# Kernel optimization log

Measured on AMD Instinct MI355X. Metric: run time of the kernel, lower is better.

The kernel has to match this reference:

```python
import jax, jax.numpy as jnp
import numpy as np

N_NODES = 100000


def gcn_conv(x, W, b, src, dst, n_nodes):
    """PyG GCNConv: add self-loops, symmetric D^-1/2 A D^-1/2 normalization,
    linear transform, gather-scale-scatter aggregation, bias."""
    h = x @ W  # [N, out]
    loops = jnp.arange(n_nodes, dtype=src.dtype)
    s = jnp.concatenate([src, loops])  # sources incl. self-loops
    d = jnp.concatenate([dst, loops])  # targets incl. self-loops
    deg = jax.ops.segment_sum(jnp.ones_like(d, dtype=h.dtype), d,
                              num_segments=n_nodes)  # in-degree (+1 self loop)
    dinv = jnp.where(deg > 0, jax.lax.rsqrt(deg), 0.0)
    norm = dinv[s] * dinv[d]  # [E+N]
    msg = h[s] * norm[:, None]  # gather + scale  [E+N, out]
    out = jax.ops.segment_sum(msg, d, num_segments=n_nodes)  # scatter-add
    return out + b


def setup_inputs() -> dict:
    key = jax.random.key(0)
    k1, k2, k3, k4, k5, k6 = jax.random.split(key, 6)
    in_ch, out_ch = 128, 64
    n_edges = 1_600_000
    x = jax.random.normal(k1, (N_NODES, in_ch), dtype=jnp.float32)
    edge_index = jax.random.randint(k2, (2, n_edges), 0, N_NODES, dtype=jnp.int64)
    # Glorot-style init for GCN weights, zero bias (PyG defaults)
    W_enc = jax.random.normal(k3, (in_ch, out_ch), dtype=jnp.float32) * (1.0 / np.sqrt(in_ch))
    b_enc = jnp.zeros((out_ch,), dtype=jnp.float32)
    W_dec = jax.random.normal(k4, (out_ch, in_ch), dtype=jnp.float32) * (1.0 / np.sqrt(out_ch))
    b_dec = jnp.zeros((in_ch,), dtype=jnp.float32)
    return {"x": x, "edge_index": edge_index,
            "W_enc": W_enc, "b_enc": b_enc, "W_dec": W_dec, "b_dec": b_dec}


def reference(x, edge_index, W_enc, b_enc, W_dec, b_dec):
    src, dst = edge_index[0], edge_index[1]
    loc_emb = gcn_conv(x, W_enc, b_enc, src, dst, N_NODES)
    loc_reconstruct = gcn_conv(loc_emb, W_dec, b_dec, src, dst, N_NODES)
    return (loc_emb, loc_reconstruct)
```

## Files before the change

kernel.cpp:

```cpp
#include <hip/hip_runtime.h>
#include <hip/hip_fp16.h>


#define BSHIFT 7
#define BNODES (1 << BSHIFT)
#define NB_LDS 1024

__global__ __launch_bounds__(1024)
void part_kernel(const int* __restrict__ src, const int* __restrict__ dst,
                 int E, int NB, int* __restrict__ gcur, int* __restrict__ gbuf,
                 int BSTRIDE)
{
    __shared__ int hist[NB_LDS];
    __shared__ int bbase[NB_LDS];
    const int tid = threadIdx.x;
    for (int i = tid; i < NB; i += 1024) hist[i] = 0;
    __syncthreads();

    const int base = (blockIdx.x * 1024 + tid) * 4;
    int bk[4], lp[4], pk[4];
    int nv = 0;
    if (base + 4 <= E) {
        const int4 d4 = *reinterpret_cast<const int4*>(dst + base);
        const int4 s4 = *reinterpret_cast<const int4*>(src + base);
        nv = 4;
        #pragma unroll
        for (int k = 0; k < 4; ++k) {
            const int d = (&d4.x)[k];
            bk[k] = d >> BSHIFT;
            pk[k] = ((&s4.x)[k] << BSHIFT) | (d & (BNODES - 1));
            lp[k] = atomicAdd(&hist[bk[k]], 1);
        }
    } else {
        for (int k = 0; base + k < E && k < 4; ++k) {
            const int d = dst[base + k];
            bk[nv] = d >> BSHIFT;
            pk[nv] = (src[base + k] << BSHIFT) | (d & (BNODES - 1));
            lp[nv] = atomicAdd(&hist[bk[nv]], 1);
            ++nv;
        }
    }
    __syncthreads();
    for (int i = tid; i < NB; i += 1024) {
        const int c = hist[i];
        bbase[i] = c ? atomicAdd(&gcur[i], c) : 0;
    }
    __syncthreads();
    for (int k = 0; k < nv; ++k) {
        const int pos = bbase[bk[k]] + lp[k];
        if (pos < BSTRIDE) gbuf[(size_t)bk[k] * BSTRIDE + pos] = pk[k];
    }
}

__global__ __launch_bounds__(256)
void csr_kernel(const int* __restrict__ gcur, const int* __restrict__ gbuf,
                int BSTRIDE, int* __restrict__ csr, int cap,
                int* __restrict__ cnt, float* __restrict__ dinv, int M)
{
    __shared__ int cur[BNODES];
    const int tid = threadIdx.x;
    const int b   = blockIdx.x;
    if (tid < BNODES) cur[tid] = 0;
    __syncthreads();

    int nb = gcur[b];
    if (nb > BSTRIDE) nb = BSTRIDE;
    const int* __restrict__ buf = gbuf + (size_t)b * BSTRIDE;
    const int n0 = b << BSHIFT;

    for (int i = tid; i < nb; i += 256) {
        const int p = buf[i];
        const int d = p & (BNODES - 1);
        const int s = p >> BSHIFT;
        const int lpos = atomicAdd(&cur[d], 1);
        if (lpos < cap) csr[(size_t)(n0 + d) * cap + lpos] = s;
    }
    __syncthreads();
    const int n = n0 + tid;
    if (tid < BNODES && n < M) {
        const int c = cur[tid];
        cnt[n]  = c;
        dinv[n] = rsqrtf((float)c + 1.0f);
    }
}

template<int K, int N, bool HOUT>
__global__ __launch_bounds__(256)
void gemm_scale(const float* __restrict__ X, const float* __restrict__ W,
                const float* __restrict__ dinv, const float* __restrict__ bias,
                float* __restrict__ out, __half* __restrict__ outh, int M)
{
    constexpr int TM  = 64;
    constexpr int QPR = K / 4;
    __shared__ float Ws[K * N];
    __shared__ float Xs[TM * K];

    const int tid  = threadIdx.x;
    const int row0 = blockIdx.x * TM;

    for (int i = tid; i < K * N / 4; i += 256) {
        float4 v = reinterpret_cast<const float4*>(W)[i];
        *reinterpret_cast<float4*>(&Ws[i * 4]) = v;
    }
    for (int i = tid; i < TM * QPR; i += 256) {
        int r = i / QPR, q = i - r * QPR;
        int gr = row0 + r;
        float4 v = make_float4(0.f, 0.f, 0.f, 0.f);
        if (gr < M) v = reinterpret_cast<const float4*>(X)[(size_t)gr * QPR + q];
        *reinterpret_cast<float4*>(&Xs[r * K + q * 4]) = v;
    }
    __syncthreads();

    constexpr int CG  = N / 4;
    constexpr int RPT = N / 16;
    const int c0 = (tid % CG) * 4;
    const int r0 = (tid / CG) * RPT;

    float a[RPT][4];
    #pragma unroll
    for (int rr = 0; rr < RPT; ++rr) {
        a[rr][0] = 0.f; a[rr][1] = 0.f; a[rr][2] = 0.f; a[rr][3] = 0.f;
    }

    #pragma unroll 4
    for (int k = 0; k < K; ++k) {
        const float4 wv = *reinterpret_cast<const float4*>(&Ws[k * N + c0]);
        #pragma unroll
        for (int rr = 0; rr < RPT; ++rr) {
            const float xv = Xs[(r0 + rr) * K + k];
            a[rr][0] += xv * wv.x;
            a[rr][1] += xv * wv.y;
            a[rr][2] += xv * wv.z;
            a[rr][3] += xv * wv.w;
        }
    }

    float4 bv = make_float4(0.f, 0.f, 0.f, 0.f);
    if (bias) bv = *reinterpret_cast<const float4*>(&bias[c0]);

    #pragma unroll
    for (int rr = 0; rr < RPT; ++rr) {
        const int gr = row0 + r0 + rr;
        if (gr < M) {
            const float d = dinv[gr];
            float4 v;
            v.x = a[rr][0] * d + bv.x; v.y = a[rr][1] * d + bv.y;
            v.z = a[rr][2] * d + bv.z; v.w = a[rr][3] * d + bv.w;
            if constexpr (HOUT) {
                union { __half2 h2[2]; uint2 u; } pk;
                pk.h2[0] = __floats2half2_rn(v.x, v.y);
                pk.h2[1] = __floats2half2_rn(v.z, v.w);
                *reinterpret_cast<uint2*>(&outh[(size_t)gr * N + c0]) = pk.u;
            } else {
                *reinterpret_cast<float4*>(&out[(size_t)gr * N + c0]) = v;
            }
        }
    }
}

template<bool FIRST>
__global__ __launch_bounds__(256)
void gcn_agg(const __half* __restrict__ hsh, const int* __restrict__ csr,
             const int* __restrict__ cnt, const float* __restrict__ dinv,
             const float* __restrict__ bias, float* __restrict__ outf,
             __half* __restrict__ outh, int M, int cap)
{
    const int lane = threadIdx.x & 63;
    int n = (blockIdx.x * 256 + threadIdx.x) >> 6;
    if (n >= M) return;
    n = __builtin_amdgcn_readfirstlane(n);
    int deg = cnt[n];
    if (deg > cap) deg = cap;
    const int* __restrict__ lst = csr + (size_t)n * cap;

    float acc = __half2float(hsh[(size_t)n * 64 + lane]);

    int j = 0;
    for (; j + 16 <= deg; j += 16) {
        int   s[16];
        float v[16];
        #pragma unroll
        for (int k = 0; k < 16; ++k) s[k] = lst[j + k];
        #pragma unroll
        for (int k = 0; k < 16; ++k) v[k] = __half2float(hsh[(size_t)s[k] * 64 + lane]);
        float t = 0.f;
        #pragma unroll
        for (int k = 0; k < 16; ++k) t += v[k];
        acc += t;
    }
    for (; j + 4 <= deg; j += 4) {
        const int s0 = lst[j], s1 = lst[j + 1], s2 = lst[j + 2], s3 = lst[j + 3];
        const float v0 = __half2float(hsh[(size_t)s0 * 64 + lane]);
        const float v1 = __half2float(hsh[(size_t)s1 * 64 + lane]);
        const float v2 = __half2float(hsh[(size_t)s2 * 64 + lane]);
        const float v3 = __half2float(hsh[(size_t)s3 * 64 + lane]);
        acc += (v0 + v1) + (v2 + v3);
    }
    for (; j < deg; ++j) acc += __half2float(hsh[(size_t)lst[j] * 64 + lane]);

    if constexpr (FIRST) {
        const float dv = dinv[n];
        const float e  = acc * dv + bias[lane];
        outf[(size_t)n * 64 + lane] = e;
        outh[(size_t)n * 64 + lane] = __float2half_rn(e * dv);
    } else {
        outf[(size_t)n * 64 + lane] = acc;
    }
}

extern "C" void kernel_launch(void* const* d_in, const int* in_sizes, int n_in,
                              void* d_out, int out_size, void* d_ws, size_t ws_size,
                              hipStream_t stream)
{
    const float* x    = (const float*)d_in[0];
    const int*   ei   = (const int*)  d_in[1];
    const float* Wenc = (const float*)d_in[2];
    const float* benc = (const float*)d_in[3];
    const float* Wdec = (const float*)d_in[4];
    const float* bdec = (const float*)d_in[5];

    const int M = in_sizes[0] / 128;
    const int E = in_sizes[1] / 2;
    const int* src  = ei;
    const int* dstv = ei + E;

    float* emb   = (float*)d_out;
    float* recon = (float*)d_out + (size_t)M * 64;

    const int NB      = (M + BNODES - 1) >> BSHIFT;
    const int BSTRIDE = 3072;

    __half* hs1h  = (__half*)d_ws;
    __half* ghalf = (__half*)((int*)d_ws + (size_t)M * 32);
    int*    gbuf  = (int*)d_ws + (size_t)M * 64;
    float*  agg2  = (float*)((int*)d_ws + (size_t)M * 64);
    int*    cnt   = (int*)d_ws + (size_t)M * 128;
    float*  dinv  = (float*)((int*)d_ws + (size_t)M * 129);
    int*    gcur  = (int*)d_ws + (size_t)M * 130;
    int*    csr   = (int*)d_ws + (size_t)M * 130 + 1024;

    const size_t used = ((size_t)M * 130 + 1024) * 4;
    int cap = 64;
    const size_t avail = (ws_size > used) ? (ws_size - used) / ((size_t)M * 4) : 0;
    if ((size_t)cap > avail) cap = (int)avail;

    hipMemsetAsync(gcur, 0, 1024 * sizeof(int), stream);

    part_kernel<<<(E + 4095) / 4096, 1024, 0, stream>>>(src, dstv, E, NB, gcur, gbuf, BSTRIDE);
    csr_kernel<<<NB, 256, 0, stream>>>(gcur, gbuf, BSTRIDE, csr, cap, cnt, dinv, M);

    const int aggBlocks = (M + 3) / 4;

    gemm_scale<128, 64, true><<<(M + 63) / 64, 256, 0, stream>>>(
        x, Wenc, dinv, nullptr, nullptr, hs1h, M);
    gcn_agg<true><<<aggBlocks, 256, 0, stream>>>(
        hs1h, csr, cnt, dinv, benc, emb, ghalf, M, cap);

    gcn_agg<false><<<aggBlocks, 256, 0, stream>>>(
        ghalf, csr, cnt, nullptr, nullptr, agg2, nullptr, M, cap);
    gemm_scale<64, 128, false><<<(M + 63) / 64, 256, 0, stream>>>(
        agg2, Wdec, dinv, bdec, recon, nullptr, M);
}
```

Measured before the change: 298.4 us.

## Register-block GEMM with 8x8 per-thread tiles and direct global X loads

```diff
diff --git a/kernel.cpp b/kernel.cpp
--- a/kernel.cpp
+++ b/kernel.cpp
@@ -84,75 +84,88 @@
     }
 }
 
-template<int K, int N, bool HOUT>
+template<int K, int N, int CG, bool HOUT>
 __global__ __launch_bounds__(256)
-void gemm_scale(const float* __restrict__ X, const float* __restrict__ W,
-                const float* __restrict__ dinv, const float* __restrict__ bias,
-                float* __restrict__ out, __half* __restrict__ outh, int M)
-{
-    constexpr int TM  = 64;
-    constexpr int QPR = K / 4;
+void gemm_rb(const float* __restrict__ X, const float* __restrict__ W,
+             const float* __restrict__ dinv, const float* __restrict__ bias,
+             float* __restrict__ out, __half* __restrict__ outh, int M)
+{
+    constexpr int RG = 256 / CG;
+    constexpr int TM = RG * 8;
     __shared__ float Ws[K * N];
-    __shared__ float Xs[TM * K];
-
-    const int tid  = threadIdx.x;
-    const int row0 = blockIdx.x * TM;
-
-    for (int i = tid; i < K * N / 4; i += 256) {
-        float4 v = reinterpret_cast<const float4*>(W)[i];
-        *reinterpret_cast<float4*>(&Ws[i * 4]) = v;
-    }
-    for (int i = tid; i < TM * QPR; i += 256) {
-        int r = i / QPR, q = i - r * QPR;
-        int gr = row0 + r;
-        float4 v = make_float4(0.f, 0.f, 0.f, 0.f);
-        if (gr < M) v = reinterpret_cast<const float4*>(X)[(size_t)gr * QPR + q];
-        *reinterpret_cast<float4*>(&Xs[r * K + q * 4]) = v;
-    }
-    __syncthreads();
-
-    constexpr int CG  = N / 4;
-    constexpr int RPT = N / 16;
-    const int c0 = (tid % CG) * 4;
-    const int r0 = (tid / CG) * RPT;
-
-    float a[RPT][4];
+
+    const int tid = threadIdx.x;
+    for (int i = tid; i < K * N / 4; i += 256)
+        reinterpret_cast<float4*>(Ws)[i] = reinterpret_cast<const float4*>(W)[i];
+    __syncthreads();
+
+    const int cg   = tid % CG;
+    const int rg   = tid / CG;
+    const int c0   = cg * 8;
+    const int row0 = blockIdx.x * TM + rg * 8;
+
+    float acc[8][8];
     #pragma unroll
-    for (int rr = 0; rr < RPT; ++rr) {
-        a[rr][0] = 0.f; a[rr][1] = 0.f; a[rr][2] = 0.f; a[rr][3] = 0.f;
-    }
-
-    #pragma unroll 4
-    for (int k = 0; k < K; ++k) {
-        const float4 wv = *reinterpret_cast<const float4*>(&Ws[k * N + c0]);
-        #pragma unroll
-        for (int rr = 0; rr < RPT; ++rr) {
-            const float xv = Xs[(r0 + rr) * K + k];
-            a[rr][0] += xv * wv.x;
-            a[rr][1] += xv * wv.y;
-            a[rr][2] += xv * wv.z;
-            a[rr][3] += xv * wv.w;
-        }
-    }
-
-    float4 bv = make_float4(0.f, 0.f, 0.f, 0.f);
-    if (bias) bv = *reinterpret_cast<const float4*>(&bias[c0]);
-
+    for (int r = 0; r < 8; ++r)
+        #pragma unroll
+        for (int c = 0; c < 8; ++c) acc[r][c] = 0.f;
+
+    const float* xp[8];
     #pragma unroll
-    for (int rr = 0; rr < RPT; ++rr) {
-        const int gr = row0 + r0 + rr;
+    for (int r = 0; r < 8; ++r) {
+        int rr = row0 + r;
+        if (rr >= M) rr = M - 1;
+        xp[r] = X + (size_t)rr * K;
+    }
+
+    for (int k = 0; k < K; k += 4) {
+        float4 xv[8];
+        #pragma unroll
+        for (int r = 0; r < 8; ++r)
+            xv[r] = *reinterpret_cast<const float4*>(xp[r] + k);
+
+        #pragma unroll
+        for (int kk = 0; kk < 4; ++kk) {
+            const float4 w0 = *reinterpret_cast<const float4*>(&Ws[(k + kk) * N + c0]);
+            const float4 w1 = *reinterpret_cast<const float4*>(&Ws[(k + kk) * N + c0 + 4]);
+            #pragma unroll
+            for (int r = 0; r < 8; ++r) {
+                const float xs = (&xv[r].x)[kk];
+                acc[r][0] += xs * w0.x; acc[r][1] += xs * w0.y;
+                acc[r][2] += xs * w0.z; acc[r][3] += xs * w0.w;
+                acc[r][4] += xs * w1.x; acc[r][5] += xs * w1.y;
+                acc[r][6] += xs * w1.z; acc[r][7] += xs * w1.w;
+            }
+        }
+    }
+
+    float4 bv0 = make_float4(0.f, 0.f, 0.f, 0.f);
+    float4 bv1 = make_float4(0.f, 0.f, 0.f, 0.f);
+    if (bias) {
+        bv0 = *reinterpret_cast<const float4*>(&bias[c0]);
+        bv1 = *reinterpret_cast<const float4*>(&bias[c0 + 4]);
+    }
+
+    #pragma unroll
+    for (int r = 0; r < 8; ++r) {
+        const int gr = row0 + r;
         if (gr < M) {
             const float d = dinv[gr];
-            float4 v;
-            v.x = a[rr][0] * d + bv.x; v.y = a[rr][1] * d + bv.y;
-            v.z = a[rr][2] * d + bv.z; v.w = a[rr][3] * d + bv.w;
             if constexpr (HOUT) {
-                union { __half2 h2[2]; uint2 u; } pk;
-                pk.h2[0] = __floats2half2_rn(v.x, v.y);
-                pk.h2[1] = __floats2half2_rn(v.z, v.w);
-                *reinterpret_cast<uint2*>(&outh[(size_t)gr * N + c0]) = pk.u;
+                union { __half2 h2[4]; uint4 u; } pk;
+                pk.h2[0] = __floats2half2_rn(acc[r][0] * d, acc[r][1] * d);
+                pk.h2[1] = __floats2half2_rn(acc[r][2] * d, acc[r][3] * d);
+                pk.h2[2] = __floats2half2_rn(acc[r][4] * d, acc[r][5] * d);
+                pk.h2[3] = __floats2half2_rn(acc[r][6] * d, acc[r][7] * d);
+                *reinterpret_cast<uint4*>(&outh[(size_t)gr * N + c0]) = pk.u;
             } else {
-                *reinterpret_cast<float4*>(&out[(size_t)gr * N + c0]) = v;
+                float4 v0, v1;
+                v0.x = acc[r][0] * d + bv0.x; v0.y = acc[r][1] * d + bv0.y;
+                v0.z = acc[r][2] * d + bv0.z; v0.w = acc[r][3] * d + bv0.w;
+                v1.x = acc[r][4] * d + bv1.x; v1.y = acc[r][5] * d + bv1.y;
+                v1.z = acc[r][6] * d + bv1.z; v1.w = acc[r][7] * d + bv1.w;
+                *reinterpret_cast<float4*>(&out[(size_t)gr * N + c0])     = v0;
+                *reinterpret_cast<float4*>(&out[(size_t)gr * N + c0 + 4]) = v1;
             }
         }
     }
@@ -251,13 +264,13 @@
 
     const int aggBlocks = (M + 3) / 4;
 
-    gemm_scale<128, 64, true><<<(M + 63) / 64, 256, 0, stream>>>(
+    gemm_rb<128, 64, 8, true><<<(M + 255) / 256, 256, 0, stream>>>(
         x, Wenc, dinv, nullptr, nullptr, hs1h, M);
     gcn_agg<true><<<aggBlocks, 256, 0, stream>>>(
         hs1h, csr, cnt, dinv, benc, emb, ghalf, M, cap);
 
     gcn_agg<false><<<aggBlocks, 256, 0, stream>>>(
         ghalf, csr, cnt, nullptr, nullptr, agg2, nullptr, M, cap);
-    gemm_scale<64, 128, false><<<(M + 63) / 64, 256, 0, stream>>>(
+    gemm_rb<64, 128, 16, false><<<(M + 127) / 128, 256, 0, stream>>>(
         agg2, Wdec, dinv, bdec, recon, nullptr, M);
 }
```

After: 295.0 us. About the same (-1.1%).

## Replace scalar FP32 LDS GEMM with FP16 MFMA matrix-core GEMM

Applied to the files above, without the earlier changes.

```diff
diff --git a/kernel.cpp b/kernel.cpp
--- a/kernel.cpp
+++ b/kernel.cpp
@@ -5,6 +5,9 @@
 #define BSHIFT 7
 #define BNODES (1 << BSHIFT)
 #define NB_LDS 1024
+
+typedef _Float16 half8 __attribute__((ext_vector_type(8)));
+typedef float    f32x4 __attribute__((ext_vector_type(4)));
 
 __global__ __launch_bounds__(1024)
 void part_kernel(const int* __restrict__ src, const int* __restrict__ dst,
@@ -86,73 +89,71 @@
 
 template<int K, int N, bool HOUT>
 __global__ __launch_bounds__(256)
-void gemm_scale(const float* __restrict__ X, const float* __restrict__ W,
-                const float* __restrict__ dinv, const float* __restrict__ bias,
-                float* __restrict__ out, __half* __restrict__ outh, int M)
-{
-    constexpr int TM  = 64;
-    constexpr int QPR = K / 4;
-    __shared__ float Ws[K * N];
-    __shared__ float Xs[TM * K];
-
-    const int tid  = threadIdx.x;
-    const int row0 = blockIdx.x * TM;
-
-    for (int i = tid; i < K * N / 4; i += 256) {
-        float4 v = reinterpret_cast<const float4*>(W)[i];
-        *reinterpret_cast<float4*>(&Ws[i * 4]) = v;
-    }
-    for (int i = tid; i < TM * QPR; i += 256) {
-        int r = i / QPR, q = i - r * QPR;
-        int gr = row0 + r;
-        float4 v = make_float4(0.f, 0.f, 0.f, 0.f);
-        if (gr < M) v = reinterpret_cast<const float4*>(X)[(size_t)gr * QPR + q];
-        *reinterpret_cast<float4*>(&Xs[r * K + q * 4]) = v;
-    }
-    __syncthreads();
-
-    constexpr int CG  = N / 4;
-    constexpr int RPT = N / 16;
-    const int c0 = (tid % CG) * 4;
-    const int r0 = (tid / CG) * RPT;
-
-    float a[RPT][4];
-    #pragma unroll
-    for (int rr = 0; rr < RPT; ++rr) {
-        a[rr][0] = 0.f; a[rr][1] = 0.f; a[rr][2] = 0.f; a[rr][3] = 0.f;
-    }
-
-    #pragma unroll 4
-    for (int k = 0; k < K; ++k) {
-        const float4 wv = *reinterpret_cast<const float4*>(&Ws[k * N + c0]);
-        #pragma unroll
-        for (int rr = 0; rr < RPT; ++rr) {
-            const float xv = Xs[(r0 + rr) * K + k];
-            a[rr][0] += xv * wv.x;
-            a[rr][1] += xv * wv.y;
-            a[rr][2] += xv * wv.z;
-            a[rr][3] += xv * wv.w;
-        }
-    }
-
-    float4 bv = make_float4(0.f, 0.f, 0.f, 0.f);
-    if (bias) bv = *reinterpret_cast<const float4*>(&bias[c0]);
-
-    #pragma unroll
-    for (int rr = 0; rr < RPT; ++rr) {
-        const int gr = row0 + r0 + rr;
-        if (gr < M) {
-            const float d = dinv[gr];
-            float4 v;
-            v.x = a[rr][0] * d + bv.x; v.y = a[rr][1] * d + bv.y;
-            v.z = a[rr][2] * d + bv.z; v.w = a[rr][3] * d + bv.w;
-            if constexpr (HOUT) {
-                union { __half2 h2[2]; uint2 u; } pk;
-                pk.h2[0] = __floats2half2_rn(v.x, v.y);
-                pk.h2[1] = __floats2half2_rn(v.z, v.w);
-                *reinterpret_cast<uint2*>(&outh[(size_t)gr * N + c0]) = pk.u;
-            } else {
-                *reinterpret_cast<float4*>(&out[(size_t)gr * N + c0]) = v;
+void gemm_mfma(const float* __restrict__ X, const float* __restrict__ W,
+               const float* __restrict__ dinv, const float* __restrict__ bias,
+               float* __restrict__ out, __half* __restrict__ outh, int M)
+{
+    constexpr int KP = K + 8;
+    constexpr int NT = N / 16;
+    constexpr int KC = K / 32;
+    __shared__ _Float16 Wt[N * KP];
+
+    const int tid = threadIdx.x;
+    for (int i = tid; i < K * N; i += 256) {
+        const int k = i / N, n = i - k * N;
+        Wt[n * KP + k] = (_Float16)W[i];
+    }
+    __syncthreads();
+
+    const int wid  = tid >> 6;
+    const int lane = tid & 63;
+    const int row0 = (blockIdx.x * 4 + wid) * 16;
+    const int rA   = lane & 15;
+    const int kg   = lane >> 4;
+
+    int ar = row0 + rA;
+    if (ar >= M) ar = M - 1;
+    const float4* __restrict__ xr4 = reinterpret_cast<const float4*>(X + (size_t)ar * K);
+
+    half8 afrag[KC];
+    #pragma unroll
+    for (int kc = 0; kc < KC; ++kc) {
+        const float4 x0 = xr4[kc * 8 + kg * 2];
+        const float4 x1 = xr4[kc * 8 + kg * 2 + 1];
+        afrag[kc][0] = (_Float16)x0.x; afrag[kc][1] = (_Float16)x0.y;
+        afrag[kc][2] = (_Float16)x0.z; afrag[kc][3] = (_Float16)x0.w;
+        afrag[kc][4] = (_Float16)x1.x; afrag[kc][5] = (_Float16)x1.y;
+        afrag[kc][6] = (_Float16)x1.z; afrag[kc][7] = (_Float16)x1.w;
+    }
+
+    f32x4 acc[NT];
+    #pragma unroll
+    for (int nt = 0; nt < NT; ++nt) acc[nt] = (f32x4){0.f, 0.f, 0.f, 0.f};
+
+    #pragma unroll
+    for (int nt = 0; nt < NT; ++nt) {
+        #pragma unroll
+        for (int kc = 0; kc < KC; ++kc) {
+            const half8 bfrag =
+                *reinterpret_cast<const half8*>(&Wt[(nt * 16 + rA) * KP + kc * 32 + kg * 8]);
+            acc[nt] = __builtin_amdgcn_mfma_f32_16x16x32_f16(afrag[kc], bfrag, acc[nt], 0, 0, 0);
+        }
+    }
+
+    const int orow0 = row0 + kg * 4;
+    #pragma unroll
+    for (int nt = 0; nt < NT; ++nt) {
+        const int col = nt * 16 + rA;
+        #pragma unroll
+        for (int r = 0; r < 4; ++r) {
+            const int gr = orow0 + r;
+            if (gr < M) {
+                const float d = dinv[gr];
+                if constexpr (HOUT) {
+                    outh[(size_t)gr * N + col] = __float2half_rn(acc[nt][r] * d);
+                } else {
+                    out[(size_t)gr * N + col] = acc[nt][r] * d + bias[col];
+                }
             }
         }
     }
@@ -251,13 +252,13 @@
 
     const int aggBlocks = (M + 3) / 4;
 
-    gemm_scale<128, 64, true><<<(M + 63) / 64, 256, 0, stream>>>(
+    gemm_mfma<128, 64, true><<<(M + 63) / 64, 256, 0, stream>>>(
         x, Wenc, dinv, nullptr, nullptr, hs1h, M);
     gcn_agg<true><<<aggBlocks, 256, 0, stream>>>(
         hs1h, csr, cnt, dinv, benc, emb, ghalf, M, cap);
 
     gcn_agg<false><<<aggBlocks, 256, 0, stream>>>(
         ghalf, csr, cnt, nullptr, nullptr, agg2, nullptr, M, cap);
-    gemm_scale<64, 128, false><<<(M + 63) / 64, 256, 0, stream>>>(
+    gemm_mfma<64, 128, false><<<(M + 63) / 64, 256, 0, stream>>>(
         agg2, Wdec, dinv, bdec, recon, nullptr, M);
 }
```

Result: faster. 271.0 us (-9.2%).
